# Kernel optimization log

Measured on AMD Instinct MI355X. Metric: run time of the kernel, lower is better.

The kernel has to match this reference:

```python
import jax, jax.numpy as jnp
import numpy as np

H = 256       # hidden_size
LAT = 32      # latent_size
AV = 40       # atom vocab size
NB = 4        # bond types
B = 256       # batch (num molecules)
LSRC = 400    # src graph length per molecule
NT = 38400    # topo predictions
NA = 38400    # atom predictions
NBD = 76800   # bond predictions


def _lin(key, fin, fout):
    k1, k2 = jax.random.split(key)
    s = 1.0 / np.sqrt(fin)
    w = jax.random.uniform(k1, (fout, fin), jnp.float32, -s, s)
    b = jax.random.uniform(k2, (fout,), jnp.float32, -s, s)
    return w, b


def setup_inputs() -> dict:
    key = jax.random.key(0)
    ks = jax.random.split(key, 24)
    d = {}
    d['src_graph_vecs'] = jax.random.normal(ks[0], (B, LSRC, LAT), jnp.float32)
    d['topo_vecs'] = jax.random.normal(ks[1], (NT, 2 * H), jnp.float32)
    d['atom_vecs'] = jax.random.normal(ks[2], (NA, 2 * H), jnp.float32)
    d['bond_vecs'] = jax.random.normal(ks[3], (NBD, 3 * H), jnp.float32)
    d['topo_idx'] = jax.random.randint(ks[4], (NT,), 0, B)
    d['atom_idx'] = jax.random.randint(ks[5], (NA,), 0, B)
    d['bond_idx'] = jax.random.randint(ks[6], (NBD,), 0, B)
    d['topo_labels'] = jax.random.randint(ks[7], (NT,), 0, 2)
    d['atom_labels'] = jax.random.randint(ks[8], (NA,), 0, AV)
    d['bond_labels'] = jax.random.randint(ks[9], (NBD,), 0, NB)
    d['A_topo_w'], d['A_topo_b'] = _lin(ks[10], 2 * H, LAT)
    d['A_atom_w'], d['A_atom_b'] = _lin(ks[11], 2 * H, LAT)
    d['A_bond_w'], d['A_bond_b'] = _lin(ks[12], 3 * H, LAT)
    d['topoNN_w1'], d['topoNN_b1'] = _lin(ks[13], 2 * H + LAT, H)
    d['topoNN_w2'], d['topoNN_b2'] = _lin(ks[14], H, 1)
    d['atomNN_w1'], d['atomNN_b1'] = _lin(ks[15], 2 * H + LAT, H)
    d['atomNN_w2'], d['atomNN_b2'] = _lin(ks[16], H, AV)
    d['bondNN_w1'], d['bondNN_b1'] = _lin(ks[17], 3 * H + LAT, H)
    d['bondNN_w2'], d['bondNN_b2'] = _lin(ks[18], H, NB)
    return d


def _attention(src, idx, q_in, Aw, Ab):
    # src: [B, L, LAT]; irregular gather per prediction row
    src_g = src[idx]                                   # [N, L, LAT]
    q = q_in @ Aw.T + Ab                               # [N, LAT]
    att = jax.nn.softmax(jnp.einsum('nld,nd->nl', src_g, q), axis=1)
    return jnp.einsum('nl,nld->nd', att, src_g)        # [N, LAT]


def _mlp(x, w1, b1, w2, b2):
    return jax.nn.relu(x @ w1.T + b1) @ w2.T + b2


def _ce_sum(logits, labels):
    lp = jax.nn.log_softmax(logits, axis=-1)
    return -jnp.sum(jnp.take_along_axis(lp, labels[:, None], axis=-1))


def reference(src_graph_vecs, topo_vecs, atom_vecs, bond_vecs,
              topo_idx, atom_idx, bond_idx,
              topo_labels, atom_labels, bond_labels,
              A_topo_w, A_topo_b, A_atom_w, A_atom_b, A_bond_w, A_bond_b,
              topoNN_w1, topoNN_b1, topoNN_w2, topoNN_b2,
              atomNN_w1, atomNN_b1, atomNN_w2, atomNN_b2,
              bondNN_w1, bondNN_b1, bondNN_w2, bondNN_b2):
    bsz = src_graph_vecs.shape[0]
    # topo head
    t_cxt = _attention(src_graph_vecs, topo_idx, topo_vecs, A_topo_w, A_topo_b)
    t_scores = _mlp(jnp.concatenate([topo_vecs, t_cxt], -1),
                    topoNN_w1, topoNN_b1, topoNN_w2, topoNN_b2)[:, 0]
    yt = topo_labels.astype(jnp.float32)
    topo_loss = jnp.sum(jax.nn.softplus(t_scores) - yt * t_scores)  # BCEWithLogits sum
    topo_acc = jnp.mean(((t_scores > 0).astype(jnp.int32) == topo_labels).astype(jnp.float32))
    # atom head
    a_cxt = _attention(src_graph_vecs, atom_idx, atom_vecs, A_atom_w, A_atom_b)
    a_scores = _mlp(jnp.concatenate([atom_vecs, a_cxt], -1),
                    atomNN_w1, atomNN_b1, atomNN_w2, atomNN_b2)
    atom_loss = _ce_sum(a_scores, atom_labels)
    atom_acc = jnp.mean((jnp.argmax(a_scores, -1) == atom_labels).astype(jnp.float32))
    # bond head
    b_cxt = _attention(src_graph_vecs, bond_idx, bond_vecs, A_bond_w, A_bond_b)
    b_scores = _mlp(jnp.concatenate([bond_vecs, b_cxt], -1),
                    bondNN_w1, bondNN_b1, bondNN_w2, bondNN_b2)
    bond_loss = _ce_sum(b_scores, bond_labels)
    bond_acc = jnp.mean((jnp.argmax(b_scores, -1) == bond_labels).astype(jnp.float32))
    loss = (topo_loss + atom_loss + bond_loss) / bsz
    return (loss, atom_acc, topo_acc, bond_acc)
```

## Files before the change

kernel.cpp:

```cpp
#include <hip/hip_runtime.h>
#include <math.h>

#define LATD 32
#define AV 40
#define NBOND 4
#define BATCH 256
#define LSRC 400
#define NT 38400
#define NA 38400
#define NBD 76800

typedef unsigned short ushort_t;
typedef short short8 __attribute__((ext_vector_type(8)));
typedef float f32x4 __attribute__((ext_vector_type(4)));
typedef unsigned short ushort4v __attribute__((ext_vector_type(4)));
typedef unsigned short ushort8v __attribute__((ext_vector_type(8)));

__device__ __forceinline__ ushort_t f2bf(float f) {
    union { float f; unsigned u; } v; v.f = f;
    unsigned r = v.u + 0x7fffu + ((v.u >> 16) & 1u);
    return (ushort_t)(r >> 16);
}
__device__ __forceinline__ float bf2f(ushort_t u) {
    union { unsigned u; float f; } v; v.u = ((unsigned)u) << 16;
    return v.f;
}

__global__ void init_kernel(float* acc, int* cnt) {
    int t = threadIdx.x;
    if (t < 8) acc[t] = 0.0f;
    cnt[t] = 0; cnt[t + 256] = 0; cnt[t + 512] = 0;
}

__global__ __launch_bounds__(256) void convbf_kernel(const float* __restrict__ in,
                                                     ushort_t* __restrict__ out, int n4) {
    int i = blockIdx.x * 256 + threadIdx.x;
    if (i < n4) {
        float4 v = ((const float4*)in)[i];
        ushort4v p;
        p[0] = f2bf(v.x); p[1] = f2bf(v.y); p[2] = f2bf(v.z); p[3] = f2bf(v.w);
        ((ushort4v*)out)[i] = p;
    }
}

__global__ __launch_bounds__(256) void hist_kernel(const int* __restrict__ idx, int N,
                                                   int* __restrict__ cnt) {
    __shared__ int lc[256];
    int t = threadIdx.x;
    lc[t] = 0;
    __syncthreads();
    for (int i = blockIdx.x * 256 + t; i < N; i += gridDim.x * 256)
        atomicAdd(&lc[idx[i]], 1);
    __syncthreads();
    if (lc[t]) atomicAdd(&cnt[t], lc[t]);
}

__global__ __launch_bounds__(256) void scan_kernel(const int* __restrict__ cnt,
                                                   int* __restrict__ cur,
                                                   int* __restrict__ bstart) {
    __shared__ int s[256];
    int t = threadIdx.x;
    for (int h = 0; h < 3; ++h) {
        int v = cnt[h * 256 + t];
        s[t] = v;
        __syncthreads();
        for (int d = 1; d < 256; d <<= 1) {
            int u = (t >= d) ? s[t - d] : 0;
            __syncthreads();
            s[t] += u;
            __syncthreads();
        }
        cur[h * 256 + t] = s[t] - v;
        bstart[h * 256 + t] = s[t] - v;
        __syncthreads();
    }
}

__global__ __launch_bounds__(256) void scatter_kernel(const int* __restrict__ idx, int N,
                                                      int* __restrict__ cur,
                                                      int* __restrict__ bucket) {
    for (int i = blockIdx.x * 256 + threadIdx.x; i < N; i += gridDim.x * 256) {
        int b = idx[i];
        int p = atomicAdd(&cur[b], 1);
        bucket[p] = i;
    }
}

template<int DIN>
__global__ __launch_bounds__(256) void qproj_kernel(
    const float* __restrict__ X,
    const float* __restrict__ Aw,
    const float* __restrict__ Ab,
    ushort_t* __restrict__ Qbf)
{
    __shared__ ushort_t As[64 * 72];
    __shared__ ushort_t Bs[32 * 72];
    const int tid = threadIdx.x;
    const int wave = tid >> 6, lane = tid & 63;
    const int l15 = lane & 15, quad = lane >> 4;
    const int row0 = blockIdx.x * 64;

    const int ar = tid >> 2;
    const int ak = (tid & 3) * 8;
    const int br = tid >> 3;
    const int bk = (tid & 7) * 8;

    f32x4 acc0 = {0.f,0.f,0.f,0.f}, acc1 = {0.f,0.f,0.f,0.f};

    for (int k0 = 0; k0 < DIN; k0 += 64) {
        {
            const float* xb = X + (size_t)(row0 + ar) * DIN + k0 + ak;
            float4 v0 = *(const float4*)xb,        v1 = *(const float4*)(xb + 4);
            float4 v2 = *(const float4*)(xb + 32), v3 = *(const float4*)(xb + 36);
            ushort8v p;
            p[0]=f2bf(v0.x); p[1]=f2bf(v0.y); p[2]=f2bf(v0.z); p[3]=f2bf(v0.w);
            p[4]=f2bf(v1.x); p[5]=f2bf(v1.y); p[6]=f2bf(v1.z); p[7]=f2bf(v1.w);
            *(ushort8v*)&As[ar * 72 + ak] = p;
            p[0]=f2bf(v2.x); p[1]=f2bf(v2.y); p[2]=f2bf(v2.z); p[3]=f2bf(v2.w);
            p[4]=f2bf(v3.x); p[5]=f2bf(v3.y); p[6]=f2bf(v3.z); p[7]=f2bf(v3.w);
            *(ushort8v*)&As[ar * 72 + ak + 32] = p;
        }
        {
            const float* wb = Aw + (size_t)br * DIN + k0 + bk;
            float4 w0 = *(const float4*)wb, w1 = *(const float4*)(wb + 4);
            ushort8v p;
            p[0]=f2bf(w0.x); p[1]=f2bf(w0.y); p[2]=f2bf(w0.z); p[3]=f2bf(w0.w);
            p[4]=f2bf(w1.x); p[5]=f2bf(w1.y); p[6]=f2bf(w1.z); p[7]=f2bf(w1.w);
            *(ushort8v*)&Bs[br * 72 + bk] = p;
        }
        __syncthreads();
        short8 a0 = *(const short8*)&As[(wave*16 + l15) * 72 + quad*8];
        short8 a1 = *(const short8*)&As[(wave*16 + l15) * 72 + 32 + quad*8];
        short8 b0 = *(const short8*)&Bs[l15 * 72 + quad*8];
        short8 b1 = *(const short8*)&Bs[l15 * 72 + 32 + quad*8];
        short8 b2 = *(const short8*)&Bs[(16 + l15) * 72 + quad*8];
        short8 b3 = *(const short8*)&Bs[(16 + l15) * 72 + 32 + quad*8];
        acc0 = __builtin_amdgcn_mfma_f32_16x16x32_bf16(a0, b0, acc0, 0, 0, 0);
        acc0 = __builtin_amdgcn_mfma_f32_16x16x32_bf16(a1, b1, acc0, 0, 0, 0);
        acc1 = __builtin_amdgcn_mfma_f32_16x16x32_bf16(a0, b2, acc1, 0, 0, 0);
        acc1 = __builtin_amdgcn_mfma_f32_16x16x32_bf16(a1, b3, acc1, 0, 0, 0);
        __syncthreads();
    }
    const float ab0 = Ab[l15];
    const float ab1 = Ab[16 + l15];
#pragma unroll
    for (int r = 0; r < 4; ++r) {
        int row = row0 + wave*16 + quad*4 + r;
        Qbf[(size_t)row * 32 + l15]      = f2bf(acc0[r] + ab0);
        Qbf[(size_t)row * 32 + 16 + l15] = f2bf(acc1[r] + ab1);
    }
}

template<int TPB, int NBLK>
__global__ __launch_bounds__(256) void attn2_kernel(
    const float* __restrict__ src,
    const ushort_t* __restrict__ Qbf,
    const int* __restrict__ bucket,
    const int* __restrict__ bstart,
    const int* __restrict__ cnt,
    ushort_t* __restrict__ cxtb)
{
    const int m  = blockIdx.x / NBLK;
    const int t0 = (blockIdx.x % NBLK) * TPB;
    const int cm = cnt[m];
    if (t0 * 32 >= cm) return;

    __shared__ __align__(16) char smem[54272];
    ushort_t* sSrcT  = (ushort_t*)(smem);
    ushort_t* sP     = (ushort_t*)(smem + 26752);
    float*    sStats = (float*)(smem + 53632);
    int*      sRows  = (int*)(smem + 54144);

    const int tid = threadIdx.x;
    const int wave = tid >> 6, lane = tid & 63;
    const int l15 = lane & 15, quad = lane >> 4;
    const int mt = wave & 1;
    const int nt = wave >> 1;
    const bool full = (nt == 0);

    {
        const float4* s4 = (const float4*)(src + (size_t)m * (LSRC * LATD));
        for (int i = tid; i < 3200; i += 256) {
            float4 v = s4[i];
            int l = i >> 3, d4 = (i & 7) * 4;
            sSrcT[(d4 + 0) * 418 + l] = f2bf(v.x);
            sSrcT[(d4 + 1) * 418 + l] = f2bf(v.y);
            sSrcT[(d4 + 2) * 418 + l] = f2bf(v.z);
            sSrcT[(d4 + 3) * 418 + l] = f2bf(v.w);
        }
        for (int i = tid; i < 512; i += 256) {
            int d = i >> 4, l = 400 + (i & 15);
            sSrcT[d * 418 + l] = 0;
        }
        for (int i = tid; i < 512; i += 256) {
            int row = i >> 4, col = 400 + (i & 15);
            sP[row * 420 + col] = 0;
        }
    }
    __syncthreads();

    const int Tm = (cm + 31) >> 5;
    const int rem = Tm - t0;
    const int ntiles = rem < TPB ? rem : TPB;

    for (int tt = 0; tt < ntiles; ++tt) {
        const int t = t0 + tt;
        if (tid < 32) {
            int p = t * 32 + tid;
            sRows[tid] = (p < cm) ? bucket[bstart[m] + p] : -1;
        }
        __syncthreads();

        const int grow = sRows[mt * 16 + l15];
        short8 aq = {0,0,0,0,0,0,0,0};
        if (grow >= 0)
            aq = *(const short8*)(Qbf + (size_t)grow * 32 + quad * 8);

        f32x4 sc[13];
#pragma unroll
        for (int j = 0; j < 13; ++j) {
            int c = nt + 2 * j;
            int bbase = quad * 8 * 418 + c * 16 + l15;
            short8 bv;
#pragma unroll
            for (int e = 0; e < 8; ++e) bv[e] = (short)sSrcT[bbase + e * 418];
            f32x4 z = {0.f, 0.f, 0.f, 0.f};
            sc[j] = __builtin_amdgcn_mfma_f32_16x16x32_bf16(aq, bv, z, 0, 0, 0);
        }

        float Mr[4], Sr[4];
#pragma unroll
        for (int r = 0; r < 4; ++r) {
            float mx = sc[0][r];
#pragma unroll
            for (int j = 1; j < 12; ++j) mx = fmaxf(mx, sc[j][r]);
            if (full) mx = fmaxf(mx, sc[12][r]);
            float s = 0.f;
#pragma unroll
            for (int j = 0; j < 12; ++j) s += __expf(sc[j][r] - mx);
            if (full) s += __expf(sc[12][r] - mx);
            Mr[r] = mx; Sr[r] = s;
        }
#pragma unroll
        for (int msk = 1; msk < 16; msk <<= 1) {
#pragma unroll
            for (int r = 0; r < 4; ++r) {
                float mo = __shfl_xor(Mr[r], msk, 64);
                float so = __shfl_xor(Sr[r], msk, 64);
                float mn = fmaxf(Mr[r], mo);
                Sr[r] = Sr[r] * __expf(Mr[r] - mn) + so * __expf(mo - mn);
                Mr[r] = mn;
            }
        }
        if (l15 == 0) {
#pragma unroll
            for (int r = 0; r < 4; ++r) {
                sStats[(wave * 16 + quad * 4 + r) * 2 + 0] = Mr[r];
                sStats[(wave * 16 + quad * 4 + r) * 2 + 1] = Sr[r];
            }
        }
        __syncthreads();
        {
            const int pw = wave ^ 2;
#pragma unroll
            for (int r = 0; r < 4; ++r) {
                float mo = sStats[(pw * 16 + quad * 4 + r) * 2 + 0];
                float so = sStats[(pw * 16 + quad * 4 + r) * 2 + 1];
                float mn = fmaxf(Mr[r], mo);
                float L = Sr[r] * __expf(Mr[r] - mn) + so * __expf(mo - mn);
                Mr[r] = mn; Sr[r] = 1.0f / L;
            }
        }
#pragma unroll
        for (int j = 0; j < 12; ++j) {
            int col = (nt + 2 * j) * 16 + l15;
#pragma unroll
            for (int r = 0; r < 4; ++r) {
                int row = mt * 16 + quad * 4 + r;
                sP[row * 420 + col] = f2bf(__expf(sc[j][r] - Mr[r]) * Sr[r]);
            }
        }
        if (full) {
            int col = 24 * 16 + l15;
#pragma unroll
            for (int r = 0; r < 4; ++r) {
                int row = mt * 16 + quad * 4 + r;
                sP[row * 420 + col] = f2bf(__expf(sc[12][r] - Mr[r]) * Sr[r]);
            }
        }
        __syncthreads();

        f32x4 oac = {0.f, 0.f, 0.f, 0.f};
#pragma unroll
        for (int k0 = 0; k0 < 416; k0 += 32) {
            short8 ap = *(const short8*)&sP[(mt * 16 + l15) * 420 + k0 + quad * 8];
            short8 bp = *(const short8*)&sSrcT[(nt * 16 + l15) * 418 + k0 + quad * 8];
            oac = __builtin_amdgcn_mfma_f32_16x16x32_bf16(ap, bp, oac, 0, 0, 0);
        }
        {
            int col = nt * 16 + l15;
#pragma unroll
            for (int r = 0; r < 4; ++r) {
                int rowl = mt * 16 + quad * 4 + r;
                int g = sRows[rowl];
                if (g >= 0) cxtb[(size_t)g * 32 + col] = f2bf(oac[r]);
            }
        }
        __syncthreads();
    }
}

template<int DIN, int DO>
__global__ __launch_bounds__(256) void mlp_mfma_kernel(
    const float* __restrict__ X,
    const ushort_t* __restrict__ cxtb,
    const ushort_t* __restrict__ W1bf,
    const float* __restrict__ B1,
    const ushort_t* __restrict__ W2bf,
    const float* __restrict__ B2,
    const int* __restrict__ labels,
    float* __restrict__ accum,
    int M)
{
    constexpr int DC = DIN + 32;
    constexpr int KITERS = DC / 32;
    constexpr int ASTR = 36;
    constexpr int HSW = 264;
    constexpr int LGW = 49;
    constexpr int NT2 = (DO + 15) / 16;

    __shared__ __align__(16) char smem[59136];
    ushort_t* As  = (ushort_t*)smem;
    ushort_t* Bs  = (ushort_t*)(smem + 4608);
    ushort_t* HS  = (ushort_t*)smem;
    ushort_t* W2s = (ushort_t*)(smem + 33792);
    float*    lg  = (float*)(smem + 33792);

    const int tid = threadIdx.x;
    const int row0 = blockIdx.x * 64;
    const int wave = tid >> 6;
    const int lane = tid & 63;
    const int l15 = lane & 15;
    const int l4 = lane >> 4;

    for (int f = tid; f < NT2 * 16 * 32; f += 256) {
        int n = f >> 5, kc = (f & 31) * 8;
        ushort8v v = (ushort8v){0,0,0,0,0,0,0,0};
        if (n < DO) v = *(const ushort8v*)&W2bf[n * 256 + kc];
        *(ushort8v*)&W2s[n * HSW + kc] = v;
    }

    f32x4 acc[4][4];
#pragma unroll
    for (int mi = 0; mi < 4; ++mi)
#pragma unroll
        for (int ni = 0; ni < 4; ++ni)
            acc[mi][ni] = (f32x4){0.f, 0.f, 0.f, 0.f};

    for (int it = 0; it < KITERS; ++it) {
        const int k0 = it * 32;
#pragma unroll
        for (int half = 0; half < 2; ++half) {
            int f = tid + half * 256;
            int row = f >> 3, k4 = (f & 7) * 4;
            ushort4v pk;
            if (k0 < DIN) {
                float4 v = *(const float4*)(X + (size_t)(row0 + row) * DIN + k0 + k4);
                pk[0] = f2bf(v.x); pk[1] = f2bf(v.y);
                pk[2] = f2bf(v.z); pk[3] = f2bf(v.w);
            } else {
                pk = *(const ushort4v*)(cxtb + (size_t)(row0 + row) * 32 + k4);
            }
            *(ushort4v*)&As[row * ASTR + k4] = pk;
        }
#pragma unroll
        for (int i = 0; i < 4; ++i) {
            int f = tid + i * 256;
            int n = f >> 2, kc = (f & 3) * 8;
            *(ushort8v*)&Bs[n * ASTR + kc] =
                *(const ushort8v*)&W1bf[(size_t)n * DC + k0 + kc];
        }
        __syncthreads();

        short8 af[4], bfv[4];
#pragma unroll
        for (int mi = 0; mi < 4; ++mi)
            af[mi] = *(const short8*)&As[(mi * 16 + l15) * ASTR + l4 * 8];
#pragma unroll
        for (int ni = 0; ni < 4; ++ni)
            bfv[ni] = *(const short8*)&Bs[(wave * 64 + ni * 16 + l15) * ASTR + l4 * 8];
#pragma unroll
        for (int mi = 0; mi < 4; ++mi)
#pragma unroll
            for (int ni = 0; ni < 4; ++ni)
                acc[mi][ni] = __builtin_amdgcn_mfma_f32_16x16x32_bf16(
                    af[mi], bfv[ni], acc[mi][ni], 0, 0, 0);
        __syncthreads();
    }

    float b1v[4];
#pragma unroll
    for (int ni = 0; ni < 4; ++ni) b1v[ni] = B1[wave * 64 + ni * 16 + l15];
#pragma unroll
    for (int mi = 0; mi < 4; ++mi) {
#pragma unroll
        for (int ni = 0; ni < 4; ++ni) {
            int col = wave * 64 + ni * 16 + l15;
#pragma unroll
            for (int r = 0; r < 4; ++r) {
                int rowl = mi * 16 + l4 * 4 + r;
                float h = fmaxf(acc[mi][ni][r] + b1v[ni], 0.0f);
                HS[rowl * HSW + col] = f2bf(h);
            }
        }
    }
    __syncthreads();

    f32x4 acc2[NT2];
#pragma unroll
    for (int nti = 0; nti < NT2; ++nti) acc2[nti] = (f32x4){0.f, 0.f, 0.f, 0.f};
#pragma unroll
    for (int kk = 0; kk < 256; kk += 32) {
        short8 af2 = *(const short8*)&HS[(wave * 16 + l15) * HSW + kk + l4 * 8];
#pragma unroll
        for (int nti = 0; nti < NT2; ++nti) {
            short8 bf2 = *(const short8*)&W2s[(nti * 16 + l15) * HSW + kk + l4 * 8];
            acc2[nti] = __builtin_amdgcn_mfma_f32_16x16x32_bf16(af2, bf2, acc2[nti], 0, 0, 0);
        }
    }
    __syncthreads();

#pragma unroll
    for (int nti = 0; nti < NT2; ++nti) {
        int col = nti * 16 + l15;
        if (col < DO) {
            float b2 = B2[col];
#pragma unroll
            for (int r = 0; r < 4; ++r)
                lg[(wave * 16 + l4 * 4 + r) * LGW + col] = acc2[nti][r] + b2;
        }
    }
    __syncthreads();

    float loss_l = 0.0f, cnt_l = 0.0f;
    if (tid < 64) {
        int lab = labels[row0 + tid];
        if (DO == 1) {
            float s = lg[tid * LGW];
            loss_l = fmaxf(s, 0.0f) + log1pf(__expf(-fabsf(s))) - (float)lab * s;
            int pred = (s > 0.0f) ? 1 : 0;
            cnt_l = (pred == lab) ? 1.0f : 0.0f;
        } else {
            const float* lr = &lg[tid * LGW];
            float mx = lr[0];
            int am = 0;
#pragma unroll
            for (int o = 1; o < DO; ++o) {
                float v = lr[o];
                if (v > mx) { mx = v; am = o; }
            }
            float se = 0.0f;
#pragma unroll
            for (int o = 0; o < DO; ++o) se += __expf(lr[o] - mx);
            loss_l = mx + logf(se) - lr[lab];
            cnt_l = (am == lab) ? 1.0f : 0.0f;
        }
#pragma unroll
        for (int off = 32; off > 0; off >>= 1) {
            loss_l += __shfl_down(loss_l, off, 64);
            cnt_l  += __shfl_down(cnt_l, off, 64);
        }
        if (tid == 0) {
            atomicAdd(accum, loss_l);
            atomicAdd(accum + 1, cnt_l);
        }
    }
}

__global__ void finalize_kernel(const float* __restrict__ acc, float* __restrict__ out) {
    if (threadIdx.x == 0) {
        out[0] = (acc[0] + acc[2] + acc[4]) / (float)BATCH;
        out[1] = acc[3] / (float)NA;
        out[2] = acc[1] / (float)NT;
        out[3] = acc[5] / (float)NBD;
    }
}

extern "C" void kernel_launch(void* const* d_in, const int* in_sizes, int n_in,
                              void* d_out, int out_size, void* d_ws, size_t ws_size,
                              hipStream_t stream) {
    const float* src      = (const float*)d_in[0];
    const float* topoX    = (const float*)d_in[1];
    const float* atomX    = (const float*)d_in[2];
    const float* bondX    = (const float*)d_in[3];
    const int*   topo_idx = (const int*)d_in[4];
    const int*   atom_idx = (const int*)d_in[5];
    const int*   bond_idx = (const int*)d_in[6];
    const int*   topo_lab = (const int*)d_in[7];
    const int*   atom_lab = (const int*)d_in[8];
    const int*   bond_lab = (const int*)d_in[9];
    const float* Atw = (const float*)d_in[10]; const float* Atb = (const float*)d_in[11];
    const float* Aaw = (const float*)d_in[12]; const float* Aab = (const float*)d_in[13];
    const float* Abw = (const float*)d_in[14]; const float* Abb = (const float*)d_in[15];
    const float* tW1 = (const float*)d_in[16]; const float* tB1 = (const float*)d_in[17];
    const float* tW2 = (const float*)d_in[18]; const float* tB2 = (const float*)d_in[19];
    const float* aW1 = (const float*)d_in[20]; const float* aB1 = (const float*)d_in[21];
    const float* aW2 = (const float*)d_in[22]; const float* aB2 = (const float*)d_in[23];
    const float* bW1 = (const float*)d_in[24]; const float* bB1 = (const float*)d_in[25];
    const float* bW2 = (const float*)d_in[26]; const float* bB2 = (const float*)d_in[27];
    float* out = (float*)d_out;

    char* ws = (char*)d_ws;
    float* acc    = (float*)ws;
    int*   cnt    = (int*)(ws + 256);
    int*   cur    = (int*)(ws + 3328);
    int*   bstart = (int*)(ws + 6400);
    int*   bkt_t  = (int*)(ws + 9472);
    int*   bkt_a  = bkt_t + NT;
    int*   bkt_b  = bkt_a + NA;
    ushort_t* cxtb = (ushort_t*)(ws + 623872);
    ushort_t* Qbf  = (ushort_t*)(ws + 5539072);
    ushort_t* w1t  = (ushort_t*)(ws + 10454272);
    ushort_t* w1a  = (ushort_t*)(ws + 10732800);
    ushort_t* w1b  = (ushort_t*)(ws + 11011328);
    ushort_t* w2t  = (ushort_t*)(ws + 11420928);
    ushort_t* w2a  = (ushort_t*)(ws + 11421440);
    ushort_t* w2b  = (ushort_t*)(ws + 11441920);

    hipLaunchKernelGGL(init_kernel, dim3(1), dim3(256), 0, stream, acc, cnt);

    hipLaunchKernelGGL(convbf_kernel, dim3((256*544/4 + 255)/256), dim3(256), 0, stream, tW1, w1t, 256*544/4);
    hipLaunchKernelGGL(convbf_kernel, dim3((256*544/4 + 255)/256), dim3(256), 0, stream, aW1, w1a, 256*544/4);
    hipLaunchKernelGGL(convbf_kernel, dim3((256*800/4 + 255)/256), dim3(256), 0, stream, bW1, w1b, 256*800/4);
    hipLaunchKernelGGL(convbf_kernel, dim3(1), dim3(256), 0, stream, tW2, w2t, 256/4);
    hipLaunchKernelGGL(convbf_kernel, dim3((40*256/4 + 255)/256), dim3(256), 0, stream, aW2, w2a, 40*256/4);
    hipLaunchKernelGGL(convbf_kernel, dim3(1), dim3(256), 0, stream, bW2, w2b, 4*256/4);

    hipLaunchKernelGGL(hist_kernel, dim3(128), dim3(256), 0, stream, topo_idx, NT, cnt + 0);
    hipLaunchKernelGGL(hist_kernel, dim3(128), dim3(256), 0, stream, atom_idx, NA, cnt + 256);
    hipLaunchKernelGGL(hist_kernel, dim3(128), dim3(256), 0, stream, bond_idx, NBD, cnt + 512);
    hipLaunchKernelGGL(scan_kernel, dim3(1), dim3(256), 0, stream, cnt, cur, bstart);
    hipLaunchKernelGGL(scatter_kernel, dim3(256), dim3(256), 0, stream, topo_idx, NT, cur + 0, bkt_t);
    hipLaunchKernelGGL(scatter_kernel, dim3(256), dim3(256), 0, stream, atom_idx, NA, cur + 256, bkt_a);
    hipLaunchKernelGGL(scatter_kernel, dim3(256), dim3(256), 0, stream, bond_idx, NBD, cur + 512, bkt_b);

    hipLaunchKernelGGL((qproj_kernel<512>), dim3(NT / 64), dim3(256), 0, stream,
                       topoX, Atw, Atb, Qbf);
    hipLaunchKernelGGL((attn2_kernel<4, 3>), dim3(256 * 3), dim3(256), 0, stream,
                       src, Qbf, bkt_t, bstart + 0, cnt + 0, cxtb);
    hipLaunchKernelGGL((mlp_mfma_kernel<512, 1>), dim3(NT / 64), dim3(256), 0, stream,
                       topoX, cxtb, w1t, tB1, w2t, tB2, topo_lab, acc + 0, NT);

    hipLaunchKernelGGL((qproj_kernel<512>), dim3(NA / 64), dim3(256), 0, stream,
                       atomX, Aaw, Aab, Qbf);
    hipLaunchKernelGGL((attn2_kernel<4, 3>), dim3(256 * 3), dim3(256), 0, stream,
                       src, Qbf, bkt_a, bstart + 256, cnt + 256, cxtb);
    hipLaunchKernelGGL((mlp_mfma_kernel<512, 40>), dim3(NA / 64), dim3(256), 0, stream,
                       atomX, cxtb, w1a, aB1, w2a, aB2, atom_lab, acc + 2, NA);

    hipLaunchKernelGGL((qproj_kernel<768>), dim3(NBD / 64), dim3(256), 0, stream,
                       bondX, Abw, Abb, Qbf);
    hipLaunchKernelGGL((attn2_kernel<5, 4>), dim3(256 * 4), dim3(256), 0, stream,
                       src, Qbf, bkt_b, bstart + 512, cnt + 512, cxtb);
    hipLaunchKernelGGL((mlp_mfma_kernel<768, 4>), dim3(NBD / 64), dim3(256), 0, stream,
                       bondX, cxtb, w1b, bB1, w2b, bB2, bond_lab, acc + 4, NBD);

    hipLaunchKernelGGL(finalize_kernel, dim3(1), dim3(64), 0, stream, acc, out);
}
```

Baseline: 1.224 ms.

## Register-prefetch next K tile in MLP kernel and read W2 from global

The first GEMM loop of the MLP kernel now prefetches the next K slice of X and W1 into registers while the MFMAs for the current slice run, so global load latency overlaps with compute. The context (cxt) slice is peeled into its own final iteration. W2 is no longer staged in shared memory; the second GEMM reads its fragments directly from global/L2. This cuts LDS use from about 59 KB to 33 KB, which should allow more blocks per CU, at the cost of higher register pressure and uncached global reads of W2 inside the inner loop.

```diff
diff --git a/kernel.cpp b/kernel.cpp
--- a/kernel.cpp
+++ b/kernel.cpp
@@ -323,18 +323,17 @@
     int M)
 {
     constexpr int DC = DIN + 32;
-    constexpr int KITERS = DC / 32;
+    constexpr int KX = DIN / 32;
     constexpr int ASTR = 36;
     constexpr int HSW = 264;
     constexpr int LGW = 49;
     constexpr int NT2 = (DO + 15) / 16;
 
-    __shared__ __align__(16) char smem[59136];
-    ushort_t* As  = (ushort_t*)smem;
-    ushort_t* Bs  = (ushort_t*)(smem + 4608);
-    ushort_t* HS  = (ushort_t*)smem;
-    ushort_t* W2s = (ushort_t*)(smem + 33792);
-    float*    lg  = (float*)(smem + 33792);
+    __shared__ __align__(16) char smem[33792];
+    ushort_t* As = (ushort_t*)smem;
+    ushort_t* Bs = (ushort_t*)(smem + 4608);
+    ushort_t* HS = (ushort_t*)smem;
+    float*    lg = (float*)smem;
 
     const int tid = threadIdx.x;
     const int row0 = blockIdx.x * 64;
@@ -343,12 +342,10 @@
     const int l15 = lane & 15;
     const int l4 = lane >> 4;
 
-    for (int f = tid; f < NT2 * 16 * 32; f += 256) {
-        int n = f >> 5, kc = (f & 31) * 8;
-        ushort8v v = (ushort8v){0,0,0,0,0,0,0,0};
-        if (n < DO) v = *(const ushort8v*)&W2bf[n * 256 + kc];
-        *(ushort8v*)&W2s[n * HSW + kc] = v;
-    }
+    const int arow = tid >> 3;
+    const int akc  = (tid & 7) * 4;
+    const int bn   = tid >> 2;
+    const int bkc  = (tid & 3) * 8;
 
     f32x4 acc[4][4];
 #pragma unroll
@@ -357,31 +354,77 @@
         for (int ni = 0; ni < 4; ++ni)
             acc[mi][ni] = (f32x4){0.f, 0.f, 0.f, 0.f};
 
-    for (int it = 0; it < KITERS; ++it) {
-        const int k0 = it * 32;
-#pragma unroll
-        for (int half = 0; half < 2; ++half) {
-            int f = tid + half * 256;
-            int row = f >> 3, k4 = (f & 7) * 4;
-            ushort4v pk;
-            if (k0 < DIN) {
-                float4 v = *(const float4*)(X + (size_t)(row0 + row) * DIN + k0 + k4);
-                pk[0] = f2bf(v.x); pk[1] = f2bf(v.y);
-                pk[2] = f2bf(v.z); pk[3] = f2bf(v.w);
-            } else {
-                pk = *(const ushort4v*)(cxtb + (size_t)(row0 + row) * 32 + k4);
-            }
-            *(ushort4v*)&As[row * ASTR + k4] = pk;
-        }
-#pragma unroll
-        for (int i = 0; i < 4; ++i) {
-            int f = tid + i * 256;
-            int n = f >> 2, kc = (f & 3) * 8;
-            *(ushort8v*)&Bs[n * ASTR + kc] =
-                *(const ushort8v*)&W1bf[(size_t)n * DC + k0 + kc];
-        }
-        __syncthreads();
-
+    float4 va0, va1;
+    ushort4v pcx0, pcx1;
+    ushort8v pb0, pb1, pb2, pb3;
+
+    va0 = *(const float4*)(X + (size_t)(row0 + arow) * DIN + akc);
+    va1 = *(const float4*)(X + (size_t)(row0 + arow + 32) * DIN + akc);
+    pb0 = *(const ushort8v*)&W1bf[(size_t)(bn)       * DC + bkc];
+    pb1 = *(const ushort8v*)&W1bf[(size_t)(bn + 64)  * DC + bkc];
+    pb2 = *(const ushort8v*)&W1bf[(size_t)(bn + 128) * DC + bkc];
+    pb3 = *(const ushort8v*)&W1bf[(size_t)(bn + 192) * DC + bkc];
+
+    for (int it = 0; it < KX; ++it) {
+        {
+            ushort4v p0, p1;
+            p0[0]=f2bf(va0.x); p0[1]=f2bf(va0.y); p0[2]=f2bf(va0.z); p0[3]=f2bf(va0.w);
+            p1[0]=f2bf(va1.x); p1[1]=f2bf(va1.y); p1[2]=f2bf(va1.z); p1[3]=f2bf(va1.w);
+            *(ushort4v*)&As[arow * ASTR + akc] = p0;
+            *(ushort4v*)&As[(arow + 32) * ASTR + akc] = p1;
+            *(ushort8v*)&Bs[(bn)       * ASTR + bkc] = pb0;
+            *(ushort8v*)&Bs[(bn + 64)  * ASTR + bkc] = pb1;
+            *(ushort8v*)&Bs[(bn + 128) * ASTR + bkc] = pb2;
+            *(ushort8v*)&Bs[(bn + 192) * ASTR + bkc] = pb3;
+        }
+        __syncthreads();
+
+        if (it + 1 < KX) {
+            const int k1 = (it + 1) * 32;
+            va0 = *(const float4*)(X + (size_t)(row0 + arow) * DIN + k1 + akc);
+            va1 = *(const float4*)(X + (size_t)(row0 + arow + 32) * DIN + k1 + akc);
+            pb0 = *(const ushort8v*)&W1bf[(size_t)(bn)       * DC + k1 + bkc];
+            pb1 = *(const ushort8v*)&W1bf[(size_t)(bn + 64)  * DC + k1 + bkc];
+            pb2 = *(const ushort8v*)&W1bf[(size_t)(bn + 128) * DC + k1 + bkc];
+            pb3 = *(const ushort8v*)&W1bf[(size_t)(bn + 192) * DC + k1 + bkc];
+        } else {
+            const int k1 = DIN;
+            pcx0 = *(const ushort4v*)(cxtb + (size_t)(row0 + arow) * 32 + akc);
+            pcx1 = *(const ushort4v*)(cxtb + (size_t)(row0 + arow + 32) * 32 + akc);
+            pb0 = *(const ushort8v*)&W1bf[(size_t)(bn)       * DC + k1 + bkc];
+            pb1 = *(const ushort8v*)&W1bf[(size_t)(bn + 64)  * DC + k1 + bkc];
+            pb2 = *(const ushort8v*)&W1bf[(size_t)(bn + 128) * DC + k1 + bkc];
+            pb3 = *(const ushort8v*)&W1bf[(size_t)(bn + 192) * DC + k1 + bkc];
+        }
+
+        {
+            short8 af[4], bfv[4];
+#pragma unroll
+            for (int mi = 0; mi < 4; ++mi)
+                af[mi] = *(const short8*)&As[(mi * 16 + l15) * ASTR + l4 * 8];
+#pragma unroll
+            for (int ni = 0; ni < 4; ++ni)
+                bfv[ni] = *(const short8*)&Bs[(wave * 64 + ni * 16 + l15) * ASTR + l4 * 8];
+#pragma unroll
+            for (int mi = 0; mi < 4; ++mi)
+#pragma unroll
+                for (int ni = 0; ni < 4; ++ni)
+                    acc[mi][ni] = __builtin_amdgcn_mfma_f32_16x16x32_bf16(
+                        af[mi], bfv[ni], acc[mi][ni], 0, 0, 0);
+        }
+        __syncthreads();
+    }
+
+    {
+        *(ushort4v*)&As[arow * ASTR + akc] = pcx0;
+        *(ushort4v*)&As[(arow + 32) * ASTR + akc] = pcx1;
+        *(ushort8v*)&Bs[(bn)       * ASTR + bkc] = pb0;
+        *(ushort8v*)&Bs[(bn + 64)  * ASTR + bkc] = pb1;
+        *(ushort8v*)&Bs[(bn + 128) * ASTR + bkc] = pb2;
+        *(ushort8v*)&Bs[(bn + 192) * ASTR + bkc] = pb3;
+    }
+    __syncthreads();
+    {
         short8 af[4], bfv[4];
 #pragma unroll
         for (int mi = 0; mi < 4; ++mi)
@@ -395,8 +438,8 @@
             for (int ni = 0; ni < 4; ++ni)
                 acc[mi][ni] = __builtin_amdgcn_mfma_f32_16x16x32_bf16(
                     af[mi], bfv[ni], acc[mi][ni], 0, 0, 0);
-        __syncthreads();
-    }
+    }
+    __syncthreads();
 
     float b1v[4];
 #pragma unroll
@@ -424,8 +467,11 @@
         short8 af2 = *(const short8*)&HS[(wave * 16 + l15) * HSW + kk + l4 * 8];
 #pragma unroll
         for (int nti = 0; nti < NT2; ++nti) {
-            short8 bf2 = *(const short8*)&W2s[(nti * 16 + l15) * HSW + kk + l4 * 8];
-            acc2[nti] = __builtin_amdgcn_mfma_f32_16x16x32_bf16(af2, bf2, acc2[nti], 0, 0, 0);
+            short8 bw = {0,0,0,0,0,0,0,0};
+            int n = nti * 16 + l15;
+            if (n < DO)
+                bw = *(const short8*)&W2bf[n * 256 + kk + l4 * 8];
+            acc2[nti] = __builtin_amdgcn_mfma_f32_16x16x32_bf16(af2, bw, acc2[nti], 0, 0, 0);
         }
     }
     __syncthreads();
```

Result: faster. 1.170 ms (-4.4%).
